# Kernel optimization log

Measured on AMD Instinct MI355X. Metric: run time of the kernel, lower is better.

Reference implementation:

```python
import jax, jax.numpy as jnp
import numpy as np

NUM_NODES = 100000
NUM_REL_P1 = 238  # num_relations + 1 (extra column for self-connection relation id -1)
B = 32768
S = 16
D_IN = 256
D_OUT = 256


def setup_inputs() -> dict:
    key = jax.random.key(0)
    k1, k2, k3, k4, k5 = jax.random.split(key, 5)
    neighbors = jax.random.randint(k1, (B, S), 0, NUM_NODES)          # sampled neighbor node ids
    relations = jax.random.randint(k2, (B, S), 0, NUM_REL_P1)          # sampled relation ids
    features = jax.random.normal(k3, (NUM_NODES, D_IN), dtype=jnp.float32)
    weight = jax.random.normal(k4, (D_OUT, D_IN), dtype=jnp.float32) * (1.0 / np.sqrt(D_IN))
    relation_weight = jax.random.normal(k5, (D_OUT, NUM_REL_P1), dtype=jnp.float32) * 0.05
    return {"neighbors": neighbors, "relations": relations, "features": features,
            "weight": weight, "relation_weight": relation_weight}


def reference(neighbors, relations, features, weight, relation_weight):
    # gather sampled neighbor embeddings: [B, S, D_in]
    neighbor_emb = features[neighbors]
    # mean-aggregate over the sample dim: [B, D_in]
    agg_neighbors = neighbor_emb.mean(axis=1)
    # linear transform: [B, D_in] @ [D_in, D_out] -> [B, D_out]
    agg_neighbors = agg_neighbors @ weight.T
    # gather + mean relation embeddings: [B, S, D_out] -> [B, D_out]
    agg_relations = relation_weight.T[relations].mean(axis=1)
    return jax.nn.relu(agg_neighbors + agg_relations)
```

## Files before the change

kernel.cpp:

```cpp
#include <hip/hip_runtime.h>

#define B_ROWS  32768
#define S_SAMP  16
#define NRELS   238
#define DIM     256
#define N_NODES 100000

typedef __attribute__((ext_vector_type(8))) short  short8;
typedef __attribute__((ext_vector_type(8))) unsigned short ushort8;
typedef __attribute__((ext_vector_type(4))) float  f32x4;

static __device__ __forceinline__ unsigned short f2bf(float f) {
    unsigned int u = __float_as_uint(f);
    u += 0x7FFFu + ((u >> 16) & 1u);
    return (unsigned short)(u >> 16);
}
static __device__ __forceinline__ float bf2f(unsigned short u) {
    return __uint_as_float(((unsigned int)u) << 16);
}

__global__ __launch_bounds__(256) void prep_kernel(const float* __restrict__ W,
                                                   const float* __restrict__ RW,
                                                   unsigned short* __restrict__ Wb,
                                                   unsigned short* __restrict__ RWTb) {
    int i = blockIdx.x * 256 + threadIdx.x;
    if (i < DIM * DIM) Wb[i] = f2bf(W[i]);
    if (i < NRELS * DIM) {
        int r = i >> 8;
        int d = i & 255;
        RWTb[i] = f2bf(RW[d * NRELS + r]);
    }
}

__global__ __launch_bounds__(512, 2) void transform_kernel(const float* __restrict__ F,
                                                           const unsigned short* __restrict__ Wb,
                                                           unsigned short* __restrict__ FT) {
    __shared__ unsigned short As[128 * 256];
    const int tid  = threadIdx.x;
    const int lane = tid & 63;
    const int wid  = tid >> 6;
    const int mg   = wid >> 2;
    const int ng   = wid & 3;
    const int col0 = lane & 15;
    const int quad = lane >> 4;

    short8 Breg[4][8];
#pragma unroll
    for (int j = 0; j < 4; ++j) {
#pragma unroll
        for (int kk = 0; kk < 8; ++kk) {
            int n = ng * 4 + j;
            Breg[j][kk] = *(const short8*)(Wb + (size_t)(n * 16 + col0) * DIM
                                              + kk * 32 + quad * 8);
        }
    }

    const int nIter = (N_NODES + 127) / 128;
    for (int it = blockIdx.x; it < nIter; it += gridDim.x) {
        const int m0 = it * 128;
#pragma unroll
        for (int i = 0; i < 8; ++i) {
            int c = i * 512 + tid;
            int r = c >> 5;
            int g = c & 31;
            int gr = m0 + r; if (gr >= N_NODES) gr = N_NODES - 1;
            const float* p = F + (size_t)gr * DIM + g * 8;
            float4 v0 = *(const float4*)p;
            float4 v1 = *(const float4*)(p + 4);
            ushort8 pk;
            pk[0] = f2bf(v0.x); pk[1] = f2bf(v0.y); pk[2] = f2bf(v0.z); pk[3] = f2bf(v0.w);
            pk[4] = f2bf(v1.x); pk[5] = f2bf(v1.y); pk[6] = f2bf(v1.z); pk[7] = f2bf(v1.w);
            int gs = g ^ (r & 7);
            *(ushort8*)&As[r * 256 + gs * 8] = pk;
        }
        __syncthreads();

#pragma unroll
        for (int mt = 0; mt < 4; ++mt) {
            const int mrow = mg * 64 + mt * 16 + col0;
            f32x4 acc[4];
#pragma unroll
            for (int j = 0; j < 4; ++j) acc[j] = (f32x4){0.f, 0.f, 0.f, 0.f};
#pragma unroll
            for (int kk = 0; kk < 8; ++kk) {
                int gs = (kk * 4 + quad) ^ (col0 & 7);
                short8 af = *(const short8*)&As[mrow * 256 + gs * 8];
#pragma unroll
                for (int j = 0; j < 4; ++j)
                    acc[j] = __builtin_amdgcn_mfma_f32_16x16x32_bf16(af, Breg[j][kk], acc[j], 0, 0, 0);
            }
            const int rbase = m0 + mg * 64 + mt * 16 + quad * 4;
#pragma unroll
            for (int j = 0; j < 4; ++j) {
                int col = (ng * 4 + j) * 16 + col0;
#pragma unroll
                for (int i2 = 0; i2 < 4; ++i2) {
                    int r = rbase + i2;
                    if (r < N_NODES) FT[(size_t)r * DIM + col] = f2bf(acc[j][i2]);
                }
            }
        }
        __syncthreads();
    }
}

__global__ __launch_bounds__(256) void aggregate_kernel(const int* __restrict__ nbr,
                                                        const int* __restrict__ rels,
                                                        const unsigned short* __restrict__ FT,
                                                        const unsigned short* __restrict__ RWTb,
                                                        float* __restrict__ out) {
    const int tid  = threadIdx.x;
    const int lane = tid & 63;
    const int row  = __builtin_amdgcn_readfirstlane(blockIdx.x * 4 + (tid >> 6));
    const int half = lane >> 5;
    const int li   = lane & 31;

    const int2* nb2 = (const int2*)(nbr  + row * S_SAMP);
    const int2* rl2 = (const int2*)(rels + row * S_SAMP);

    float acc[8] = {0.f, 0.f, 0.f, 0.f, 0.f, 0.f, 0.f, 0.f};
#pragma unroll
    for (int t = 0; t < 8; ++t) {
        int2 nn = nb2[t];
        int2 rr = rl2[t];
        int nid = half ? nn.y : nn.x;
        int rid = half ? rr.y : rr.x;
        ushort8 f = *(const ushort8*)(FT   + (size_t)nid * DIM + li * 8);
        ushort8 g = *(const ushort8*)(RWTb + (size_t)rid * DIM + li * 8);
#pragma unroll
        for (int j = 0; j < 8; ++j) acc[j] += bf2f(f[j]) + bf2f(g[j]);
    }
#pragma unroll
    for (int j = 0; j < 8; ++j) acc[j] += __shfl_xor(acc[j], 32, 64);

    const float sc = 1.0f / 16.0f;
    float s0 = half ? acc[4] : acc[0];
    float s1 = half ? acc[5] : acc[1];
    float s2 = half ? acc[6] : acc[2];
    float s3 = half ? acc[7] : acc[3];
    float4 o;
    o.x = fmaxf(s0 * sc, 0.f);
    o.y = fmaxf(s1 * sc, 0.f);
    o.z = fmaxf(s2 * sc, 0.f);
    o.w = fmaxf(s3 * sc, 0.f);
    *(float4*)(out + (size_t)row * DIM + li * 8 + half * 4) = o;
}

extern "C" void kernel_launch(void* const* d_in, const int* in_sizes, int n_in,
                              void* d_out, int out_size, void* d_ws, size_t ws_size,
                              hipStream_t stream) {
    const int*   neighbors = (const int*)d_in[0];
    const int*   relations = (const int*)d_in[1];
    const float* features  = (const float*)d_in[2];
    const float* weight    = (const float*)d_in[3];
    const float* relw      = (const float*)d_in[4];
    float* out = (float*)d_out;

    char* ws = (char*)d_ws;
    unsigned short* Wb   = (unsigned short*)ws;
    unsigned short* RWTb = (unsigned short*)(ws + 131072);
    unsigned short* FT   = (unsigned short*)(ws + 253952);

    prep_kernel<<<256, 256, 0, stream>>>(weight, relw, Wb, RWTb);
    transform_kernel<<<256, 512, 0, stream>>>(features, Wb, FT);
    aggregate_kernel<<<B_ROWS / 4, 256, 0, stream>>>(neighbors, relations, FT, RWTb, out);
}
```

Measured before the change: 228.9 us.

## Aggregate neighbors before the linear transform and fuse gather with MFMA GEMM

Reorders the computation so that neighbor features are gathered and mean-aggregated first, and the weight matrix is applied only to the B aggregated rows rather than all N nodes. The GEMM, relation-embedding add and ReLU are fused into one kernel per 32-row tile. The full feature table is still converted to bf16 in a streaming prep kernel, which replaces the old transform kernel. This removes about two thirds of the matmul FLOPs. In exchange it adds a bf16 rounding of the aggregated means before the GEMM, and each block reloads the weight fragments into registers.

```diff
diff --git a/kernel.cpp b/kernel.cpp
--- a/kernel.cpp
+++ b/kernel.cpp
@@ -5,9 +5,10 @@
 #define NRELS   238
 #define DIM     256
 #define N_NODES 100000
+#define NF4     ((N_NODES * DIM) / 4)
+#define CONV_BLOCKS (NF4 / 256)
 
 typedef __attribute__((ext_vector_type(8))) short  short8;
-typedef __attribute__((ext_vector_type(8))) unsigned short ushort8;
 typedef __attribute__((ext_vector_type(4))) float  f32x4;
 
 static __device__ __forceinline__ unsigned short f2bf(float f) {
@@ -19,131 +20,119 @@
     return __uint_as_float(((unsigned int)u) << 16);
 }
 
-__global__ __launch_bounds__(256) void prep_kernel(const float* __restrict__ W,
+__global__ __launch_bounds__(256) void prep_kernel(const float* __restrict__ F,
+                                                   const float* __restrict__ W,
                                                    const float* __restrict__ RW,
+                                                   unsigned short* __restrict__ Fb,
                                                    unsigned short* __restrict__ Wb,
                                                    unsigned short* __restrict__ RWTb) {
-    int i = blockIdx.x * 256 + threadIdx.x;
-    if (i < DIM * DIM) Wb[i] = f2bf(W[i]);
-    if (i < NRELS * DIM) {
-        int r = i >> 8;
-        int d = i & 255;
-        RWTb[i] = f2bf(RW[d * NRELS + r]);
+    if (blockIdx.x < CONV_BLOCKS) {
+        int i = blockIdx.x * 256 + threadIdx.x;
+        float4 v = ((const float4*)F)[i];
+        ushort4 p;
+        p.x = f2bf(v.x); p.y = f2bf(v.y); p.z = f2bf(v.z); p.w = f2bf(v.w);
+        ((ushort4*)Fb)[i] = p;
+    } else {
+        int i = (blockIdx.x - CONV_BLOCKS) * 256 + threadIdx.x;
+        if (i < DIM * DIM) Wb[i] = f2bf(W[i]);
+        if (i < NRELS * DIM) {
+            int r = i >> 8;
+            int d = i & 255;
+            RWTb[i] = f2bf(RW[d * NRELS + r]);
+        }
     }
 }
 
-__global__ __launch_bounds__(512, 2) void transform_kernel(const float* __restrict__ F,
-                                                           const unsigned short* __restrict__ Wb,
-                                                           unsigned short* __restrict__ FT) {
-    __shared__ unsigned short As[128 * 256];
+__global__ __launch_bounds__(256) void fused_kernel(const int* __restrict__ nbr,
+                                                    const int* __restrict__ rels,
+                                                    const unsigned short* __restrict__ Fb,
+                                                    const unsigned short* __restrict__ RWTb,
+                                                    const unsigned short* __restrict__ Wb,
+                                                    float* __restrict__ out) {
+    __shared__ unsigned short As[32][264];
+    __shared__ unsigned short Rs[32][264];
     const int tid  = threadIdx.x;
     const int lane = tid & 63;
-    const int wid  = tid >> 6;
-    const int mg   = wid >> 2;
-    const int ng   = wid & 3;
+    const int wid  = __builtin_amdgcn_readfirstlane(tid >> 6);
     const int col0 = lane & 15;
     const int quad = lane >> 4;
+    const int r0g  = blockIdx.x * 32;
+
+    const float sc = 1.0f / 16.0f;
+    for (int i = 0; i < 8; ++i) {
+        const int row_l = wid * 8 + i;
+        const int row_g = r0g + row_l;
+        const int2* nb2 = (const int2*)(nbr  + row_g * S_SAMP);
+        const int2* rl2 = (const int2*)(rels + row_g * S_SAMP);
+        float a0 = 0.f, a1 = 0.f, a2 = 0.f, a3 = 0.f;
+        float b0 = 0.f, b1 = 0.f, b2 = 0.f, b3 = 0.f;
+#pragma unroll
+        for (int t = 0; t < 8; ++t) {
+            int2 nn = nb2[t];
+            int2 rr = rl2[t];
+            ushort4 f0 = *(const ushort4*)(Fb   + (size_t)nn.x * DIM + lane * 4);
+            ushort4 g0 = *(const ushort4*)(RWTb + (size_t)rr.x * DIM + lane * 4);
+            ushort4 f1 = *(const ushort4*)(Fb   + (size_t)nn.y * DIM + lane * 4);
+            ushort4 g1 = *(const ushort4*)(RWTb + (size_t)rr.y * DIM + lane * 4);
+            a0 += bf2f(f0.x) + bf2f(f1.x);
+            a1 += bf2f(f0.y) + bf2f(f1.y);
+            a2 += bf2f(f0.z) + bf2f(f1.z);
+            a3 += bf2f(f0.w) + bf2f(f1.w);
+            b0 += bf2f(g0.x) + bf2f(g1.x);
+            b1 += bf2f(g0.y) + bf2f(g1.y);
+            b2 += bf2f(g0.z) + bf2f(g1.z);
+            b3 += bf2f(g0.w) + bf2f(g1.w);
+        }
+        ushort4 pa, pr;
+        pa.x = f2bf(a0 * sc); pa.y = f2bf(a1 * sc); pa.z = f2bf(a2 * sc); pa.w = f2bf(a3 * sc);
+        pr.x = f2bf(b0 * sc); pr.y = f2bf(b1 * sc); pr.z = f2bf(b2 * sc); pr.w = f2bf(b3 * sc);
+        *(ushort4*)&As[row_l][lane * 4] = pa;
+        *(ushort4*)&Rs[row_l][lane * 4] = pr;
+    }
 
     short8 Breg[4][8];
 #pragma unroll
     for (int j = 0; j < 4; ++j) {
 #pragma unroll
         for (int kk = 0; kk < 8; ++kk) {
-            int n = ng * 4 + j;
+            int n = wid * 4 + j;
             Breg[j][kk] = *(const short8*)(Wb + (size_t)(n * 16 + col0) * DIM
                                               + kk * 32 + quad * 8);
         }
     }
+    __syncthreads();
 
-    const int nIter = (N_NODES + 127) / 128;
-    for (int it = blockIdx.x; it < nIter; it += gridDim.x) {
-        const int m0 = it * 128;
+    f32x4 acc[2][4];
 #pragma unroll
-        for (int i = 0; i < 8; ++i) {
-            int c = i * 512 + tid;
-            int r = c >> 5;
-            int g = c & 31;
-            int gr = m0 + r; if (gr >= N_NODES) gr = N_NODES - 1;
-            const float* p = F + (size_t)gr * DIM + g * 8;
-            float4 v0 = *(const float4*)p;
-            float4 v1 = *(const float4*)(p + 4);
-            ushort8 pk;
-            pk[0] = f2bf(v0.x); pk[1] = f2bf(v0.y); pk[2] = f2bf(v0.z); pk[3] = f2bf(v0.w);
-            pk[4] = f2bf(v1.x); pk[5] = f2bf(v1.y); pk[6] = f2bf(v1.z); pk[7] = f2bf(v1.w);
-            int gs = g ^ (r & 7);
-            *(ushort8*)&As[r * 256 + gs * 8] = pk;
-        }
-        __syncthreads();
+    for (int mt = 0; mt < 2; ++mt)
+#pragma unroll
+        for (int j = 0; j < 4; ++j) acc[mt][j] = (f32x4){0.f, 0.f, 0.f, 0.f};
 
 #pragma unroll
-        for (int mt = 0; mt < 4; ++mt) {
-            const int mrow = mg * 64 + mt * 16 + col0;
-            f32x4 acc[4];
+    for (int mt = 0; mt < 2; ++mt) {
+        const int mrow = mt * 16 + col0;
 #pragma unroll
-            for (int j = 0; j < 4; ++j) acc[j] = (f32x4){0.f, 0.f, 0.f, 0.f};
+        for (int kk = 0; kk < 8; ++kk) {
+            short8 af = *(const short8*)&As[mrow][kk * 32 + quad * 8];
 #pragma unroll
-            for (int kk = 0; kk < 8; ++kk) {
-                int gs = (kk * 4 + quad) ^ (col0 & 7);
-                short8 af = *(const short8*)&As[mrow * 256 + gs * 8];
+            for (int j = 0; j < 4; ++j)
+                acc[mt][j] = __builtin_amdgcn_mfma_f32_16x16x32_bf16(af, Breg[j][kk], acc[mt][j], 0, 0, 0);
+        }
+    }
+
 #pragma unroll
-                for (int j = 0; j < 4; ++j)
-                    acc[j] = __builtin_amdgcn_mfma_f32_16x16x32_bf16(af, Breg[j][kk], acc[j], 0, 0, 0);
-            }
-            const int rbase = m0 + mg * 64 + mt * 16 + quad * 4;
+    for (int mt = 0; mt < 2; ++mt) {
 #pragma unroll
-            for (int j = 0; j < 4; ++j) {
-                int col = (ng * 4 + j) * 16 + col0;
+        for (int j = 0; j < 4; ++j) {
+            const int col = (wid * 4 + j) * 16 + col0;
 #pragma unroll
-                for (int i2 = 0; i2 < 4; ++i2) {
-                    int r = rbase + i2;
-                    if (r < N_NODES) FT[(size_t)r * DIM + col] = f2bf(acc[j][i2]);
-                }
+            for (int i2 = 0; i2 < 4; ++i2) {
+                const int r_l = mt * 16 + quad * 4 + i2;
+                float v = acc[mt][j][i2] + bf2f(Rs[r_l][col]);
+                out[(size_t)(r0g + r_l) * DIM + col] = v > 0.f ? v : 0.f;
             }
         }
-        __syncthreads();
     }
-}
-
-__global__ __launch_bounds__(256) void aggregate_kernel(const int* __restrict__ nbr,
-                                                        const int* __restrict__ rels,
-                                                        const unsigned short* __restrict__ FT,
-                                                        const unsigned short* __restrict__ RWTb,
-                                                        float* __restrict__ out) {
-    const int tid  = threadIdx.x;
-    const int lane = tid & 63;
-    const int row  = __builtin_amdgcn_readfirstlane(blockIdx.x * 4 + (tid >> 6));
-    const int half = lane >> 5;
-    const int li   = lane & 31;
-
-    const int2* nb2 = (const int2*)(nbr  + row * S_SAMP);
-    const int2* rl2 = (const int2*)(rels + row * S_SAMP);
-
-    float acc[8] = {0.f, 0.f, 0.f, 0.f, 0.f, 0.f, 0.f, 0.f};
-#pragma unroll
-    for (int t = 0; t < 8; ++t) {
-        int2 nn = nb2[t];
-        int2 rr = rl2[t];
-        int nid = half ? nn.y : nn.x;
-        int rid = half ? rr.y : rr.x;
-        ushort8 f = *(const ushort8*)(FT   + (size_t)nid * DIM + li * 8);
-        ushort8 g = *(const ushort8*)(RWTb + (size_t)rid * DIM + li * 8);
-#pragma unroll
-        for (int j = 0; j < 8; ++j) acc[j] += bf2f(f[j]) + bf2f(g[j]);
-    }
-#pragma unroll
-    for (int j = 0; j < 8; ++j) acc[j] += __shfl_xor(acc[j], 32, 64);
-
-    const float sc = 1.0f / 16.0f;
-    float s0 = half ? acc[4] : acc[0];
-    float s1 = half ? acc[5] : acc[1];
-    float s2 = half ? acc[6] : acc[2];
-    float s3 = half ? acc[7] : acc[3];
-    float4 o;
-    o.x = fmaxf(s0 * sc, 0.f);
-    o.y = fmaxf(s1 * sc, 0.f);
-    o.z = fmaxf(s2 * sc, 0.f);
-    o.w = fmaxf(s3 * sc, 0.f);
-    *(float4*)(out + (size_t)row * DIM + li * 8 + half * 4) = o;
 }
 
 extern "C" void kernel_launch(void* const* d_in, const int* in_sizes, int n_in,
@@ -159,9 +148,8 @@
     char* ws = (char*)d_ws;
     unsigned short* Wb   = (unsigned short*)ws;
     unsigned short* RWTb = (unsigned short*)(ws + 131072);
-    unsigned short* FT   = (unsigned short*)(ws + 253952);
+    unsigned short* Fb   = (unsigned short*)(ws + 253952);
 
-    prep_kernel<<<256, 256, 0, stream>>>(weight, relw, Wb, RWTb);
-    transform_kernel<<<256, 512, 0, stream>>>(features, Wb, FT);
-    aggregate_kernel<<<B_ROWS / 4, 256, 0, stream>>>(neighbors, relations, FT, RWTb, out);
+    prep_kernel<<<CONV_BLOCKS + 256, 256, 0, stream>>>(features, weight, relw, Fb, Wb, RWTb);
+    fused_kernel<<<B_ROWS / 32, 256, 0, stream>>>(neighbors, relations, Fb, RWTb, Wb, out);
 }
```

After: 240.9 us. +5.2%, slower.
